# Kernel tuning notes

Measured on AMD Instinct MI355X. Metric: run time of the kernel, lower is better.

## Reference

```python
import jax, jax.numpy as jnp
import numpy as np

N_NODES = 10000
N_EDGES = 320000
IN_DIM = 256
HID = 64
HEADS = 4
OUT_DIM = 64
NEG_SLOPE = 0.2


def setup_inputs() -> dict:
    key = jax.random.key(0)
    ks = jax.random.split(key, 10)
    s = 0.05
    return {
        "h": jax.random.normal(ks[0], (N_NODES, IN_DIM), jnp.float32),
        "src": jax.random.randint(ks[1], (N_EDGES,), 0, N_NODES, jnp.int32),
        "dst": jax.random.randint(ks[2], (N_EDGES,), 0, N_NODES, jnp.int32),
        "W1": jax.random.normal(ks[3], (IN_DIM, HEADS * HID), jnp.float32) * s,
        "al1": jax.random.normal(ks[4], (HEADS, HID), jnp.float32) * s,
        "ar1": jax.random.normal(ks[5], (HEADS, HID), jnp.float32) * s,
        "b1": jnp.zeros((HEADS * HID,), jnp.float32),
        "W2": jax.random.normal(ks[6], (HEADS * HID, OUT_DIM), jnp.float32) * s,
        "al2": jax.random.normal(ks[7], (1, OUT_DIM), jnp.float32) * s,
        "ar2": jax.random.normal(ks[8], (1, OUT_DIM), jnp.float32) * s,
        "b2": jnp.zeros((OUT_DIM,), jnp.float32),
    }


def _gatconv(h, W, al, ar, b, src, dst, n_heads, d_out):
    """DGL-style GATConv: project, edge-softmax attention, scatter-aggregate."""
    n = h.shape[0]
    feat = (h @ W).reshape(n, n_heads, d_out)          # [N,H,D]
    el = jnp.sum(feat * al, axis=-1)                   # [N,H]
    er = jnp.sum(feat * ar, axis=-1)                   # [N,H]
    e = jax.nn.leaky_relu(el[src] + er[dst], NEG_SLOPE)  # [E,H]
    # segment softmax over incoming edges of each dst node
    m = jax.ops.segment_max(e, dst, num_segments=n)    # [N,H]
    ex = jnp.exp(e - m[dst])                           # [E,H]
    denom = jax.ops.segment_sum(ex, dst, num_segments=n)  # [N,H]
    alpha = ex / denom[dst]                            # [E,H]
    msg = feat[src] * alpha[:, :, None]                # [E,H,D]
    out = jax.ops.segment_sum(msg, dst, num_segments=n)  # [N,H,D]
    return out + b.reshape(n_heads, d_out)


def reference(h, src, dst, W1, al1, ar1, b1, W2, al2, ar2, b2):
    h1 = _gatconv(h, W1, al1, ar1, b1, src, dst, HEADS, HID)
    h1 = jax.nn.elu(h1.reshape(N_NODES, HEADS * HID))  # flatten(1) then ELU
    h2 = _gatconv(h1, W2, al2, ar2, b2, src, dst, 1, OUT_DIM)
    return jnp.squeeze(h2, axis=1)  # [N, OUT_DIM]
```

## Files before the change

kernel.cpp:

```cpp
#include <hip/hip_runtime.h>
#include <hip/hip_bf16.h>
#include <stdint.h>

#define NN 10000
#define NE 320000
#define NH 4
#define BCAP 128

#define GEMM1_MB 79
#define GEMM1_BLOCKS (GEMM1_MB * 4)
#define BUILD_BLOCKS 1250

typedef __attribute__((ext_vector_type(8))) short s16x8;
typedef __attribute__((ext_vector_type(4))) float f32x4;
typedef __attribute__((ext_vector_type(8))) unsigned short u16x8;

static __device__ __forceinline__ float b2f(unsigned short u) {
    union { unsigned int i; float f; } x; x.i = ((unsigned int)u) << 16; return x.f;
}
static __device__ __forceinline__ unsigned short f2b(float f) {
    unsigned int u = __float_as_uint(f);
    unsigned int r = (u + 0x7fffu + ((u >> 16) & 1u)) >> 16;
    return (unsigned short)r;
}

__global__ __launch_bounds__(256) void k_prep(const unsigned short* __restrict__ hraw,
                        const void* __restrict__ W1, const void* __restrict__ W2,
                        const void* al1, const void* ar1, const void* b1,
                        const void* al2, const void* ar2, const void* b2,
                        unsigned short* __restrict__ W1T, unsigned short* __restrict__ W2T,
                        unsigned short* __restrict__ canon, int* __restrict__ cnt,
                        int* __restrict__ flag) {
    __shared__ int sb[256];
    int t = threadIdx.x;
    int c = 0;
    for (int i = t; i < 2048; i += 256) {
        unsigned short u = hraw[i];
        int e = (u >> 7) & 0xFF;
        c += (e >= 97 && e <= 157) ? 1 : 0;
    }
    sb[t] = c;
    __syncthreads();
    for (int o = 128; o > 0; o >>= 1) {
        if (t < o) sb[t] += sb[t + o];
        __syncthreads();
    }
    int isbf = (sb[0] >= 1741) ? 1 : 0;

    int idx = blockIdx.x * 256 + t;
    if (idx < 65536) {
        int n = idx >> 8, k = idx & 255;
        W1T[idx] = isbf ? ((const unsigned short*)W1)[k * 256 + n]
                        : f2b(((const float*)W1)[k * 256 + n]);
    } else if (idx < 81920) {
        int j = idx - 65536;
        int n = j >> 8, k = j & 255;
        W2T[j] = isbf ? ((const unsigned short*)W2)[k * 64 + n]
                      : f2b(((const float*)W2)[k * 64 + n]);
    } else if (idx < 82880) {
        int j = idx - 81920;
        const void* srcp; int q;
        if      (j < 256) { srcp = al1; q = j; }
        else if (j < 512) { srcp = ar1; q = j - 256; }
        else if (j < 768) { srcp = b1;  q = j - 512; }
        else if (j < 832) { srcp = al2; q = j - 768; }
        else if (j < 896) { srcp = ar2; q = j - 832; }
        else              { srcp = b2;  q = j - 896; }
        canon[j] = isbf ? ((const unsigned short*)srcp)[q] : f2b(((const float*)srcp)[q]);
    } else if (idx < 92880) {
        cnt[idx - 82880] = 0;
    } else if (idx == 92880) {
        flag[0] = isbf;
    }
}

#define BSTRIDE 264
static __device__ __forceinline__ void gemm_body(short* Bs,
                        const void* __restrict__ A, const unsigned short* __restrict__ BT,
                        unsigned short* __restrict__ C,
                        float* __restrict__ el, float* __restrict__ er,
                        const unsigned short* __restrict__ al,
                        const unsigned short* __restrict__ ar,
                        int M, int N, int H, int a_isbf, int mtile, int head) {
    int t = threadIdx.x;
    int wave = t >> 6, lane = t & 63;
    int m0 = mtile * 128;
    const unsigned short* Bh = BT + (size_t)head * 64 * 256;

#pragma unroll
    for (int i = 0; i < 8; ++i) {
        int idx = t + i * 256;
        int row = idx >> 5, chunk = idx & 31;
        *(s16x8*)&Bs[row * BSTRIDE + chunk * 8] =
            *(const s16x8*)&Bh[(size_t)row * 256 + chunk * 8];
    }
    __syncthreads();

    int kq = (lane >> 4) * 8;
    const unsigned short* Ab = (const unsigned short*)A;
    const float*          Af = (const float*)A;
    int aR[2];
#pragma unroll
    for (int mi = 0; mi < 2; ++mi) {
        int aRow = m0 + mi * 64 + wave * 16 + (lane & 15);
        aR[mi] = (aRow < M) ? aRow : M - 1;
    }
    f32x4 acc[2][4] = {};

#pragma unroll
    for (int k0 = 0; k0 < 256; k0 += 32) {
        s16x8 afr[2];
#pragma unroll
        for (int mi = 0; mi < 2; ++mi) {
            if (a_isbf) {
                afr[mi] = *(const s16x8*)&Ab[(size_t)aR[mi] * 256 + k0 + kq];
            } else {
                const float* pf = &Af[(size_t)aR[mi] * 256 + k0 + kq];
                float4 x0 = *(const float4*)pf;
                float4 x1 = *(const float4*)(pf + 4);
                afr[mi][0] = (short)f2b(x0.x); afr[mi][1] = (short)f2b(x0.y);
                afr[mi][2] = (short)f2b(x0.z); afr[mi][3] = (short)f2b(x0.w);
                afr[mi][4] = (short)f2b(x1.x); afr[mi][5] = (short)f2b(x1.y);
                afr[mi][6] = (short)f2b(x1.z); afr[mi][7] = (short)f2b(x1.w);
            }
        }
#pragma unroll
        for (int nt = 0; nt < 4; ++nt) {
            s16x8 bfr = *(const s16x8*)&Bs[(nt * 16 + (lane & 15)) * BSTRIDE + k0 + kq];
            acc[0][nt] = __builtin_amdgcn_mfma_f32_16x16x32_bf16(afr[0], bfr, acc[0][nt], 0, 0, 0);
            acc[1][nt] = __builtin_amdgcn_mfma_f32_16x16x32_bf16(afr[1], bfr, acc[1][nt], 0, 0, 0);
        }
    }

    float alv[4], arv[4];
#pragma unroll
    for (int nt = 0; nt < 4; ++nt) {
        int c = (lane & 15) + nt * 16;
        alv[nt] = b2f(al[head * 64 + c]);
        arv[nt] = b2f(ar[head * 64 + c]);
    }
    int col0 = head * 64 + (lane & 15);
#pragma unroll
    for (int mi = 0; mi < 2; ++mi) {
        int r0 = m0 + mi * 64 + wave * 16 + (lane >> 4) * 4;
        float cr[4][4];
#pragma unroll
        for (int nt = 0; nt < 4; ++nt) {
            int col = col0 + nt * 16;
#pragma unroll
            for (int i = 0; i < 4; ++i) {
                unsigned short cb = f2b(acc[mi][nt][i]);
                cr[nt][i] = b2f(cb);
                int r = r0 + i;
                if (r < M) C[(size_t)r * N + col] = cb;
            }
        }
#pragma unroll
        for (int i = 0; i < 4; ++i) {
            float pl = 0.f, pr = 0.f;
#pragma unroll
            for (int nt = 0; nt < 4; ++nt) {
                pl += cr[nt][i] * alv[nt];
                pr += cr[nt][i] * arv[nt];
            }
#pragma unroll
            for (int o = 1; o < 16; o <<= 1) {
                pl += __shfl_xor(pl, o, 64);
                pr += __shfl_xor(pr, o, 64);
            }
            int r = r0 + i;
            if ((lane & 15) == 0 && r < M) {
                el[(size_t)r * H + head] = pl;
                er[(size_t)r * H + head] = pr;
            }
        }
    }
}

__global__ __launch_bounds__(256) void k_g1b(const void* __restrict__ A,
                        const unsigned short* __restrict__ W1T,
                        unsigned short* __restrict__ feat1,
                        float* __restrict__ el, float* __restrict__ er,
                        const unsigned short* __restrict__ al,
                        const unsigned short* __restrict__ ar,
                        const int* __restrict__ flagp,
                        const int* __restrict__ src, const int* __restrict__ dst,
                        int* __restrict__ cnt, int* __restrict__ bucket) {
    __shared__ short Bs[64 * BSTRIDE];
    int bid = blockIdx.x;
    if (bid < GEMM1_BLOCKS) {
        int head = bid / GEMM1_MB;
        int mtile = bid - head * GEMM1_MB;
        gemm_body(Bs, A, W1T, feat1, el, er, al, ar, NN, 256, NH, flagp[0], mtile, head);
    } else {
        int i = (bid - GEMM1_BLOCKS) * 256 + threadIdx.x;
        if (i < NE) {
            int d = dst[i];
            int pos = atomicAdd(&cnt[d], 1);
            if (pos < BCAP) bucket[(d << 7) + pos] = src[i];
        }
    }
}

__global__ __launch_bounds__(256) void k_gemm(const void* __restrict__ A,
                                              const unsigned short* __restrict__ BT,
                                              unsigned short* __restrict__ C,
                                              float* __restrict__ el, float* __restrict__ er,
                                              const unsigned short* __restrict__ al,
                                              const unsigned short* __restrict__ ar,
                                              int M, int N, int H) {
    __shared__ short Bs[64 * BSTRIDE];
    gemm_body(Bs, A, BT, C, el, er, al, ar, M, N, H, 1, blockIdx.x, blockIdx.y);
}

__global__ __launch_bounds__(256) void k_edge1(const int* __restrict__ cnt,
                        const int* __restrict__ bucket,
                        const float* __restrict__ el, const float* __restrict__ er,
                        const unsigned short* __restrict__ feat,
                        const unsigned short* __restrict__ b1,
                        unsigned short* __restrict__ h1) {
    int wave = threadIdx.x >> 6, lane = threadIdx.x & 63;
    int node = blockIdx.x * 4 + wave;
    if (node >= NN) return;
    int eg = lane >> 3, d8 = lane & 7;
    int end = cnt[node]; if (end > BCAP) end = BCAP;
    const int* bkt = bucket + ((size_t)node << 7);
    float4 er4 = *(const float4*)&er[(size_t)node * 4];

    if (end <= 64) {
        int s = 0;
        float w0 = 0.f, w1 = 0.f, w2 = 0.f, w3 = 0.f;
        if (lane < end) {
            s = bkt[lane];
            float4 el4 = *(const float4*)&el[(size_t)s * 4];
            float x0 = el4.x + er4.x; x0 = (x0 >= 0.f) ? x0 : 0.2f * x0;
            float x1 = el4.y + er4.y; x1 = (x1 >= 0.f) ? x1 : 0.2f * x1;
            float x2 = el4.z + er4.z; x2 = (x2 >= 0.f) ? x2 : 0.2f * x2;
            float x3 = el4.w + er4.w; x3 = (x3 >= 0.f) ? x3 : 0.2f * x3;
            w0 = __expf(x0); w1 = __expf(x1);
            w2 = __expf(x2); w3 = __expf(x3);
        }
        int niter = (end + 7) >> 3;
#pragma unroll
        for (int h = 0; h < 4; ++h) {
            float wh = (h == 0) ? w0 : (h == 1) ? w1 : (h == 2) ? w2 : w3;
            float a[8] = {};
            for (int i = 0; i < niter; ++i) {
                int idx = 8 * i + eg;
                float we = __shfl(wh, idx, 64);
                int   se = __shfl(s, idx, 64);
                u16x8 fv = *(const u16x8*)&feat[(((size_t)se * NH + h) << 6) + (d8 << 3)];
#pragma unroll
                for (int j = 0; j < 8; ++j) a[j] += we * b2f(fv[j]);
            }
            float ls = wh;
#pragma unroll
            for (int o = 1; o < 64; o <<= 1) ls += __shfl_xor(ls, o, 64);
#pragma unroll
            for (int j = 0; j < 8; ++j) {
                a[j] += __shfl_xor(a[j], 8, 64);
                a[j] += __shfl_xor(a[j], 16, 64);
                a[j] += __shfl_xor(a[j], 32, 64);
            }
            if (eg == 0) {
                float inv = (ls > 0.f) ? 1.f / ls : 0.f;
                u16x8 r;
#pragma unroll
                for (int j = 0; j < 8; ++j) {
                    float o = a[j] * inv + b2f(b1[h * 64 + d8 * 8 + j]);
                    o = (o > 0.f) ? o : (__expf(o) - 1.f);
                    r[j] = f2b(o);
                }
                *(u16x8*)&h1[(((size_t)node * NH + h) << 6) + d8 * 8] = r;
            }
        }
    } else {
        float a[4][8] = {};
        float ls0 = 0.f, ls1 = 0.f, ls2 = 0.f, ls3 = 0.f;
        for (int base = 0; base < end; base += 64) {
            int c = base + lane;
            int s = 0;
            float w0 = 0.f, w1 = 0.f, w2 = 0.f, w3 = 0.f;
            if (c < end) {
                s = bkt[c];
                float4 el4 = *(const float4*)&el[(size_t)s * 4];
                float x0 = el4.x + er4.x; x0 = (x0 >= 0.f) ? x0 : 0.2f * x0;
                float x1 = el4.y + er4.y; x1 = (x1 >= 0.f) ? x1 : 0.2f * x1;
                float x2 = el4.z + er4.z; x2 = (x2 >= 0.f) ? x2 : 0.2f * x2;
                float x3 = el4.w + er4.w; x3 = (x3 >= 0.f) ? x3 : 0.2f * x3;
                w0 = __expf(x0); w1 = __expf(x1);
                w2 = __expf(x2); w3 = __expf(x3);
            }
            ls0 += w0; ls1 += w1; ls2 += w2; ls3 += w3;
            int cn = end - base; if (cn > 64) cn = 64;
            int niter = (cn + 7) >> 3;
#pragma unroll
            for (int h = 0; h < 4; ++h) {
                float wh = (h == 0) ? w0 : (h == 1) ? w1 : (h == 2) ? w2 : w3;
                for (int i = 0; i < niter; ++i) {
                    int idx = 8 * i + eg;
                    float we = __shfl(wh, idx, 64);
                    int   se = __shfl(s, idx, 64);
                    u16x8 fv = *(const u16x8*)&feat[(((size_t)se * NH + h) << 6) + (d8 << 3)];
#pragma unroll
                    for (int j = 0; j < 8; ++j) a[h][j] += we * b2f(fv[j]);
                }
            }
        }
#pragma unroll
        for (int h = 0; h < 4; ++h) {
            float ls = (h == 0) ? ls0 : (h == 1) ? ls1 : (h == 2) ? ls2 : ls3;
#pragma unroll
            for (int o = 1; o < 64; o <<= 1) ls += __shfl_xor(ls, o, 64);
#pragma unroll
            for (int j = 0; j < 8; ++j) {
                a[h][j] += __shfl_xor(a[h][j], 8, 64);
                a[h][j] += __shfl_xor(a[h][j], 16, 64);
                a[h][j] += __shfl_xor(a[h][j], 32, 64);
            }
            if (eg == 0) {
                float inv = (ls > 0.f) ? 1.f / ls : 0.f;
                u16x8 r;
#pragma unroll
                for (int j = 0; j < 8; ++j) {
                    float o = a[h][j] * inv + b2f(b1[h * 64 + d8 * 8 + j]);
                    o = (o > 0.f) ? o : (__expf(o) - 1.f);
                    r[j] = f2b(o);
                }
                *(u16x8*)&h1[(((size_t)node * NH + h) << 6) + d8 * 8] = r;
            }
        }
    }
}

__global__ __launch_bounds__(256) void k_edge2(const int* __restrict__ cnt,
                        const int* __restrict__ bucket,
                        const float* __restrict__ el, const float* __restrict__ er,
                        const unsigned short* __restrict__ feat,
                        const unsigned short* __restrict__ b2,
                        void* __restrict__ out, const int* __restrict__ flagp) {
    int wave = threadIdx.x >> 6, lane = threadIdx.x & 63;
    int node = blockIdx.x * 4 + wave;
    if (node >= NN) return;
    int eg = lane >> 3, d8 = lane & 7;
    int isbf = flagp[0];
    int end = cnt[node]; if (end > BCAP) end = BCAP;
    const int* bkt = bucket + ((size_t)node << 7);
    float er_d = er[node];
    float lsum = 0.f;
    float a[8] = {};
    for (int base = 0; base < end; base += 64) {
        int c = base + lane;
        float wgt = 0.f; int s = 0;
        if (c < end) {
            s = bkt[c];
            float x = el[s] + er_d;
            x = (x >= 0.f) ? x : 0.2f * x;
            wgt = __expf(x);
        }
        lsum += wgt;
        int cn = end - base; if (cn > 64) cn = 64;
        int niter = (cn + 7) >> 3;
#pragma unroll 2
        for (int i = 0; i < niter; ++i) {
            int idx = 8 * i + eg;
            float we = __shfl(wgt, idx, 64);
            int   se = __shfl(s, idx, 64);
            u16x8 fv = *(const u16x8*)&feat[((size_t)se << 6) + (d8 << 3)];
#pragma unroll
            for (int j = 0; j < 8; ++j) a[j] += we * b2f(fv[j]);
        }
    }
#pragma unroll
    for (int o = 1; o < 64; o <<= 1) lsum += __shfl_xor(lsum, o, 64);
#pragma unroll
    for (int j = 0; j < 8; ++j) {
        a[j] += __shfl_xor(a[j], 8, 64);
        a[j] += __shfl_xor(a[j], 16, 64);
        a[j] += __shfl_xor(a[j], 32, 64);
    }
    if (eg == 0) {
        float inv = (lsum > 0.f) ? 1.f / lsum : 0.f;
        float o[8];
#pragma unroll
        for (int j = 0; j < 8; ++j) o[j] = a[j] * inv + b2f(b2[d8 * 8 + j]);
        size_t ob = ((size_t)node << 6) + d8 * 8;
        if (isbf) {
            u16x8 r;
#pragma unroll
            for (int j = 0; j < 8; ++j) r[j] = f2b(o[j]);
            *(u16x8*)&((unsigned short*)out)[ob] = r;
        } else {
            float4 r0, r1;
            r0.x = o[0]; r0.y = o[1]; r0.z = o[2]; r0.w = o[3];
            r1.x = o[4]; r1.y = o[5]; r1.z = o[6]; r1.w = o[7];
            *(float4*)&((float*)out)[ob] = r0;
            *(float4*)&((float*)out)[ob + 4] = r1;
        }
    }
}

extern "C" void kernel_launch(void* const* d_in, const int* in_sizes, int n_in,
                              void* d_out, int out_size, void* d_ws, size_t ws_size,
                              hipStream_t stream) {
    const void* h   = d_in[0];
    const int*  src = (const int*)d_in[1];
    const int*  dst = (const int*)d_in[2];
    const void* W1  = d_in[3];
    const void* al1 = d_in[4];
    const void* ar1 = d_in[5];
    const void* b1  = d_in[6];
    const void* W2  = d_in[7];
    const void* al2 = d_in[8];
    const void* ar2 = d_in[9];
    const void* b2  = d_in[10];

    char* w = (char*)d_ws;
    size_t off = 0;
    auto alloc = [&](size_t bytes) -> void* {
        void* p = w + off;
        off = (off + bytes + 255) & ~(size_t)255;
        return p;
    };
    int* flag               = (int*)alloc(8);
    int* cnt                = (int*)alloc(NN * 4);
    int* bucket             = (int*)alloc((size_t)NN * BCAP * 4);
    unsigned short* canon   = (unsigned short*)alloc(960 * 2);
    unsigned short* W1T     = (unsigned short*)alloc(256 * 256 * 2);
    unsigned short* W2T     = (unsigned short*)alloc(64 * 256 * 2);
    unsigned short* feat1   = (unsigned short*)alloc((size_t)NN * 256 * 2);
    float* el1              = (float*)alloc(NN * NH * 4);
    float* er1              = (float*)alloc(NN * NH * 4);
    unsigned short* h1      = (unsigned short*)alloc((size_t)NN * 256 * 2);
    unsigned short* feat2   = (unsigned short*)alloc((size_t)NN * 64 * 2);
    float* el2              = (float*)alloc(NN * 4);
    float* er2              = (float*)alloc(NN * 4);
    (void)ws_size; (void)in_sizes; (void)n_in; (void)out_size;

    unsigned short* cal1 = canon + 0;
    unsigned short* car1 = canon + 256;
    unsigned short* cb1  = canon + 512;
    unsigned short* cal2 = canon + 768;
    unsigned short* car2 = canon + 832;
    unsigned short* cb2  = canon + 896;

    k_prep<<<363, 256, 0, stream>>>((const unsigned short*)h, W1, W2,
                                    al1, ar1, b1, al2, ar2, b2,
                                    W1T, W2T, canon, cnt, flag);
    k_g1b<<<GEMM1_BLOCKS + BUILD_BLOCKS, 256, 0, stream>>>(h, W1T, feat1, el1, er1,
                                                           cal1, car1, flag,
                                                           src, dst, cnt, bucket);
    k_edge1<<<(NN + 3) / 4, 256, 0, stream>>>(cnt, bucket, el1, er1, feat1, cb1, h1);
    k_gemm<<<dim3(GEMM1_MB, 1), 256, 0, stream>>>(h1, W2T, feat2, el2, er2,
                                                  cal2, car2, NN, 64, 1);
    k_edge2<<<(NN + 3) / 4, 256, 0, stream>>>(cnt, bucket, el2, er2, feat2, cb2, d_out, flag);
}
```

Before: 157.9 us.

## Split layer-1 aggregation per head and halve GEMM row tiles for more parallelism

Replaces the per-node layer-1 edge kernel, which looped over all four heads in one wave, with a kernel that launches one wave per (node, head) pair, giving four times as many waves and fewer accumulator registers per wave. The GEMM tile shrinks from 128 to 64 rows, doubling the block count for both GEMMs. The layer-2 edge kernel gains a single-chunk fast path for nodes with at most 64 incoming edges, plus occupancy hints. In exchange, each edge's source index and per-edge weight are now computed once per head instead of once per node, and el/er are read with a stride of four floats.

```diff
diff --git a/kernel.cpp b/kernel.cpp
--- a/kernel.cpp
+++ b/kernel.cpp
@@ -7,8 +7,8 @@
 #define NH 4
 #define BCAP 128
 
-#define GEMM1_MB 79
-#define GEMM1_BLOCKS (GEMM1_MB * 4)
+#define GEMM1_MT 157
+#define GEMM1_BLOCKS (GEMM1_MT * 4)
 #define BUILD_BLOCKS 1250
 
 typedef __attribute__((ext_vector_type(8))) short s16x8;
@@ -84,7 +84,7 @@
                         int M, int N, int H, int a_isbf, int mtile, int head) {
     int t = threadIdx.x;
     int wave = t >> 6, lane = t & 63;
-    int m0 = mtile * 128;
+    int m0 = mtile * 64;
     const unsigned short* Bh = BT + (size_t)head * 64 * 256;
 
 #pragma unroll
@@ -99,36 +99,28 @@
     int kq = (lane >> 4) * 8;
     const unsigned short* Ab = (const unsigned short*)A;
     const float*          Af = (const float*)A;
-    int aR[2];
-#pragma unroll
-    for (int mi = 0; mi < 2; ++mi) {
-        int aRow = m0 + mi * 64 + wave * 16 + (lane & 15);
-        aR[mi] = (aRow < M) ? aRow : M - 1;
-    }
-    f32x4 acc[2][4] = {};
+    int aRow = m0 + wave * 16 + (lane & 15);
+    int aR = (aRow < M) ? aRow : M - 1;
+    f32x4 acc[4] = {};
 
 #pragma unroll
     for (int k0 = 0; k0 < 256; k0 += 32) {
-        s16x8 afr[2];
-#pragma unroll
-        for (int mi = 0; mi < 2; ++mi) {
-            if (a_isbf) {
-                afr[mi] = *(const s16x8*)&Ab[(size_t)aR[mi] * 256 + k0 + kq];
-            } else {
-                const float* pf = &Af[(size_t)aR[mi] * 256 + k0 + kq];
-                float4 x0 = *(const float4*)pf;
-                float4 x1 = *(const float4*)(pf + 4);
-                afr[mi][0] = (short)f2b(x0.x); afr[mi][1] = (short)f2b(x0.y);
-                afr[mi][2] = (short)f2b(x0.z); afr[mi][3] = (short)f2b(x0.w);
-                afr[mi][4] = (short)f2b(x1.x); afr[mi][5] = (short)f2b(x1.y);
-                afr[mi][6] = (short)f2b(x1.z); afr[mi][7] = (short)f2b(x1.w);
-            }
+        s16x8 afr;
+        if (a_isbf) {
+            afr = *(const s16x8*)&Ab[(size_t)aR * 256 + k0 + kq];
+        } else {
+            const float* pf = &Af[(size_t)aR * 256 + k0 + kq];
+            float4 x0 = *(const float4*)pf;
+            float4 x1 = *(const float4*)(pf + 4);
+            afr[0] = (short)f2b(x0.x); afr[1] = (short)f2b(x0.y);
+            afr[2] = (short)f2b(x0.z); afr[3] = (short)f2b(x0.w);
+            afr[4] = (short)f2b(x1.x); afr[5] = (short)f2b(x1.y);
+            afr[6] = (short)f2b(x1.z); afr[7] = (short)f2b(x1.w);
         }
 #pragma unroll
         for (int nt = 0; nt < 4; ++nt) {
             s16x8 bfr = *(const s16x8*)&Bs[(nt * 16 + (lane & 15)) * BSTRIDE + k0 + kq];
-            acc[0][nt] = __builtin_amdgcn_mfma_f32_16x16x32_bf16(afr[0], bfr, acc[0][nt], 0, 0, 0);
-            acc[1][nt] = __builtin_amdgcn_mfma_f32_16x16x32_bf16(afr[1], bfr, acc[1][nt], 0, 0, 0);
+            acc[nt] = __builtin_amdgcn_mfma_f32_16x16x32_bf16(afr, bfr, acc[nt], 0, 0, 0);
         }
     }
 
@@ -140,39 +132,36 @@
         arv[nt] = b2f(ar[head * 64 + c]);
     }
     int col0 = head * 64 + (lane & 15);
-#pragma unroll
-    for (int mi = 0; mi < 2; ++mi) {
-        int r0 = m0 + mi * 64 + wave * 16 + (lane >> 4) * 4;
-        float cr[4][4];
+    int r0 = m0 + wave * 16 + (lane >> 4) * 4;
+    float cr[4][4];
+#pragma unroll
+    for (int nt = 0; nt < 4; ++nt) {
+        int col = col0 + nt * 16;
+#pragma unroll
+        for (int i = 0; i < 4; ++i) {
+            unsigned short cb = f2b(acc[nt][i]);
+            cr[nt][i] = b2f(cb);
+            int r = r0 + i;
+            if (r < M) C[(size_t)r * N + col] = cb;
+        }
+    }
+#pragma unroll
+    for (int i = 0; i < 4; ++i) {
+        float pl = 0.f, pr = 0.f;
 #pragma unroll
         for (int nt = 0; nt < 4; ++nt) {
-            int col = col0 + nt * 16;
-#pragma unroll
-            for (int i = 0; i < 4; ++i) {
-                unsigned short cb = f2b(acc[mi][nt][i]);
-                cr[nt][i] = b2f(cb);
-                int r = r0 + i;
-                if (r < M) C[(size_t)r * N + col] = cb;
-            }
-        }
-#pragma unroll
-        for (int i = 0; i < 4; ++i) {
-            float pl = 0.f, pr = 0.f;
-#pragma unroll
-            for (int nt = 0; nt < 4; ++nt) {
-                pl += cr[nt][i] * alv[nt];
-                pr += cr[nt][i] * arv[nt];
-            }
-#pragma unroll
-            for (int o = 1; o < 16; o <<= 1) {
-                pl += __shfl_xor(pl, o, 64);
-                pr += __shfl_xor(pr, o, 64);
-            }
-            int r = r0 + i;
-            if ((lane & 15) == 0 && r < M) {
-                el[(size_t)r * H + head] = pl;
-                er[(size_t)r * H + head] = pr;
-            }
+            pl += cr[nt][i] * alv[nt];
+            pr += cr[nt][i] * arv[nt];
+        }
+#pragma unroll
+        for (int o = 1; o < 16; o <<= 1) {
+            pl += __shfl_xor(pl, o, 64);
+            pr += __shfl_xor(pr, o, 64);
+        }
+        int r = r0 + i;
+        if ((lane & 15) == 0 && r < M) {
+            el[(size_t)r * H + head] = pl;
+            er[(size_t)r * H + head] = pr;
         }
     }
 }
@@ -189,8 +178,8 @@
     __shared__ short Bs[64 * BSTRIDE];
     int bid = blockIdx.x;
     if (bid < GEMM1_BLOCKS) {
-        int head = bid / GEMM1_MB;
-        int mtile = bid - head * GEMM1_MB;
+        int head = bid / GEMM1_MT;
+        int mtile = bid - head * GEMM1_MT;
         gemm_body(Bs, A, W1T, feat1, el, er, al, ar, NN, 256, NH, flagp[0], mtile, head);
     } else {
         int i = (bid - GEMM1_BLOCKS) * 256 + threadIdx.x;
@@ -198,6 +187,107 @@
             int d = dst[i];
             int pos = atomicAdd(&cnt[d], 1);
             if (pos < BCAP) bucket[(d << 7) + pos] = src[i];
+        }
+    }
+}
+
+__global__ __launch_bounds__(256, 8) void k_e1h(const int* __restrict__ cnt,
+                        const int* __restrict__ bucket,
+                        const float* __restrict__ el, const float* __restrict__ er,
+                        const unsigned short* __restrict__ feat,
+                        const unsigned short* __restrict__ b1,
+                        unsigned short* __restrict__ h1) {
+    int wave = threadIdx.x >> 6, lane = threadIdx.x & 63;
+    int bid = blockIdx.x;
+    int head = bid / 2500;
+    int node = (bid - head * 2500) * 4 + wave;
+    int eg = lane >> 3, d8 = lane & 7;
+    int end = cnt[node]; if (end > BCAP) end = BCAP;
+    const int* bkt = bucket + ((size_t)node << 7);
+    float er_d = er[(size_t)node * 4 + head];
+
+    if (end <= 64) {
+        int s = 0; float w = 0.f;
+        if (lane < end) {
+            s = bkt[lane];
+            float x = el[(size_t)s * 4 + head] + er_d;
+            x = (x >= 0.f) ? x : 0.2f * x;
+            w = __expf(x);
+        }
+        float ls = w;
+#pragma unroll
+        for (int o = 1; o < 64; o <<= 1) ls += __shfl_xor(ls, o, 64);
+        float a[8] = {};
+        int niter = (end + 7) >> 3;
+#pragma unroll 4
+        for (int i = 0; i < niter; ++i) {
+            int idx = 8 * i + eg;
+            int   se = __shfl(s, idx, 64);
+            float we = __shfl(w, idx, 64);
+            u16x8 fv = *(const u16x8*)&feat[(((size_t)se * NH + head) << 6) + (d8 << 3)];
+#pragma unroll
+            for (int j = 0; j < 8; ++j) a[j] += we * b2f(fv[j]);
+        }
+#pragma unroll
+        for (int j = 0; j < 8; ++j) {
+            a[j] += __shfl_xor(a[j], 8, 64);
+            a[j] += __shfl_xor(a[j], 16, 64);
+            a[j] += __shfl_xor(a[j], 32, 64);
+        }
+        if (eg == 0) {
+            float inv = (ls > 0.f) ? 1.f / ls : 0.f;
+            u16x8 r;
+#pragma unroll
+            for (int j = 0; j < 8; ++j) {
+                float o = a[j] * inv + b2f(b1[head * 64 + d8 * 8 + j]);
+                o = (o > 0.f) ? o : (__expf(o) - 1.f);
+                r[j] = f2b(o);
+            }
+            *(u16x8*)&h1[(((size_t)node * NH + head) << 6) + d8 * 8] = r;
+        }
+    } else {
+        float a[8] = {};
+        float ls = 0.f;
+        for (int base = 0; base < end; base += 64) {
+            int c = base + lane;
+            int s = 0; float w = 0.f;
+            if (c < end) {
+                s = bkt[c];
+                float x = el[(size_t)s * 4 + head] + er_d;
+                x = (x >= 0.f) ? x : 0.2f * x;
+                w = __expf(x);
+            }
+            ls += w;
+            int cn = end - base; if (cn > 64) cn = 64;
+            int niter = (cn + 7) >> 3;
+#pragma unroll 2
+            for (int i = 0; i < niter; ++i) {
+                int idx = 8 * i + eg;
+                int   se = __shfl(s, idx, 64);
+                float we = __shfl(w, idx, 64);
+                u16x8 fv = *(const u16x8*)&feat[(((size_t)se * NH + head) << 6) + (d8 << 3)];
+#pragma unroll
+                for (int j = 0; j < 8; ++j) a[j] += we * b2f(fv[j]);
+            }
+        }
+#pragma unroll
+        for (int o = 1; o < 64; o <<= 1) ls += __shfl_xor(ls, o, 64);
+#pragma unroll
+        for (int j = 0; j < 8; ++j) {
+            a[j] += __shfl_xor(a[j], 8, 64);
+            a[j] += __shfl_xor(a[j], 16, 64);
+            a[j] += __shfl_xor(a[j], 32, 64);
+        }
+        if (eg == 0) {
+            float inv = (ls > 0.f) ? 1.f / ls : 0.f;
+            u16x8 r;
+#pragma unroll
+            for (int j = 0; j < 8; ++j) {
+                float o = a[j] * inv + b2f(b1[head * 64 + d8 * 8 + j]);
+                o = (o > 0.f) ? o : (__expf(o) - 1.f);
+                r[j] = f2b(o);
+            }
+            *(u16x8*)&h1[(((size_t)node * NH + head) << 6) + d8 * 8] = r;
         }
     }
 }
@@ -213,127 +303,7 @@
     gemm_body(Bs, A, BT, C, el, er, al, ar, M, N, H, 1, blockIdx.x, blockIdx.y);
 }
 
-__global__ __launch_bounds__(256) void k_edge1(const int* __restrict__ cnt,
-                        const int* __restrict__ bucket,
-                        const float* __restrict__ el, const float* __restrict__ er,
-                        const unsigned short* __restrict__ feat,
-                        const unsigned short* __restrict__ b1,
-                        unsigned short* __restrict__ h1) {
-    int wave = threadIdx.x >> 6, lane = threadIdx.x & 63;
-    int node = blockIdx.x * 4 + wave;
-    if (node >= NN) return;
-    int eg = lane >> 3, d8 = lane & 7;
-    int end = cnt[node]; if (end > BCAP) end = BCAP;
-    const int* bkt = bucket + ((size_t)node << 7);
-    float4 er4 = *(const float4*)&er[(size_t)node * 4];
-
-    if (end <= 64) {
-        int s = 0;
-        float w0 = 0.f, w1 = 0.f, w2 = 0.f, w3 = 0.f;
-        if (lane < end) {
-            s = bkt[lane];
-            float4 el4 = *(const float4*)&el[(size_t)s * 4];
-            float x0 = el4.x + er4.x; x0 = (x0 >= 0.f) ? x0 : 0.2f * x0;
-            float x1 = el4.y + er4.y; x1 = (x1 >= 0.f) ? x1 : 0.2f * x1;
-            float x2 = el4.z + er4.z; x2 = (x2 >= 0.f) ? x2 : 0.2f * x2;
-            float x3 = el4.w + er4.w; x3 = (x3 >= 0.f) ? x3 : 0.2f * x3;
-            w0 = __expf(x0); w1 = __expf(x1);
-            w2 = __expf(x2); w3 = __expf(x3);
-        }
-        int niter = (end + 7) >> 3;
-#pragma unroll
-        for (int h = 0; h < 4; ++h) {
-            float wh = (h == 0) ? w0 : (h == 1) ? w1 : (h == 2) ? w2 : w3;
-            float a[8] = {};
-            for (int i = 0; i < niter; ++i) {
-                int idx = 8 * i + eg;
-                float we = __shfl(wh, idx, 64);
-                int   se = __shfl(s, idx, 64);
-                u16x8 fv = *(const u16x8*)&feat[(((size_t)se * NH + h) << 6) + (d8 << 3)];
-#pragma unroll
-                for (int j = 0; j < 8; ++j) a[j] += we * b2f(fv[j]);
-            }
-            float ls = wh;
-#pragma unroll
-            for (int o = 1; o < 64; o <<= 1) ls += __shfl_xor(ls, o, 64);
-#pragma unroll
-            for (int j = 0; j < 8; ++j) {
-                a[j] += __shfl_xor(a[j], 8, 64);
-                a[j] += __shfl_xor(a[j], 16, 64);
-                a[j] += __shfl_xor(a[j], 32, 64);
-            }
-            if (eg == 0) {
-                float inv = (ls > 0.f) ? 1.f / ls : 0.f;
-                u16x8 r;
-#pragma unroll
-                for (int j = 0; j < 8; ++j) {
-                    float o = a[j] * inv + b2f(b1[h * 64 + d8 * 8 + j]);
-                    o = (o > 0.f) ? o : (__expf(o) - 1.f);
-                    r[j] = f2b(o);
-                }
-                *(u16x8*)&h1[(((size_t)node * NH + h) << 6) + d8 * 8] = r;
-            }
-        }
-    } else {
-        float a[4][8] = {};
-        float ls0 = 0.f, ls1 = 0.f, ls2 = 0.f, ls3 = 0.f;
-        for (int base = 0; base < end; base += 64) {
-            int c = base + lane;
-            int s = 0;
-            float w0 = 0.f, w1 = 0.f, w2 = 0.f, w3 = 0.f;
-            if (c < end) {
-                s = bkt[c];
-                float4 el4 = *(const float4*)&el[(size_t)s * 4];
-                float x0 = el4.x + er4.x; x0 = (x0 >= 0.f) ? x0 : 0.2f * x0;
-                float x1 = el4.y + er4.y; x1 = (x1 >= 0.f) ? x1 : 0.2f * x1;
-                float x2 = el4.z + er4.z; x2 = (x2 >= 0.f) ? x2 : 0.2f * x2;
-                float x3 = el4.w + er4.w; x3 = (x3 >= 0.f) ? x3 : 0.2f * x3;
-                w0 = __expf(x0); w1 = __expf(x1);
-                w2 = __expf(x2); w3 = __expf(x3);
-            }
-            ls0 += w0; ls1 += w1; ls2 += w2; ls3 += w3;
-            int cn = end - base; if (cn > 64) cn = 64;
-            int niter = (cn + 7) >> 3;
-#pragma unroll
-            for (int h = 0; h < 4; ++h) {
-                float wh = (h == 0) ? w0 : (h == 1) ? w1 : (h == 2) ? w2 : w3;
-                for (int i = 0; i < niter; ++i) {
-                    int idx = 8 * i + eg;
-                    float we = __shfl(wh, idx, 64);
-                    int   se = __shfl(s, idx, 64);
-                    u16x8 fv = *(const u16x8*)&feat[(((size_t)se * NH + h) << 6) + (d8 << 3)];
-#pragma unroll
-                    for (int j = 0; j < 8; ++j) a[h][j] += we * b2f(fv[j]);
-                }
-            }
-        }
-#pragma unroll
-        for (int h = 0; h < 4; ++h) {
-            float ls = (h == 0) ? ls0 : (h == 1) ? ls1 : (h == 2) ? ls2 : ls3;
-#pragma unroll
-            for (int o = 1; o < 64; o <<= 1) ls += __shfl_xor(ls, o, 64);
-#pragma unroll
-            for (int j = 0; j < 8; ++j) {
-                a[h][j] += __shfl_xor(a[h][j], 8, 64);
-                a[h][j] += __shfl_xor(a[h][j], 16, 64);
-                a[h][j] += __shfl_xor(a[h][j], 32, 64);
-            }
-            if (eg == 0) {
-                float inv = (ls > 0.f) ? 1.f / ls : 0.f;
-                u16x8 r;
-#pragma unroll
-                for (int j = 0; j < 8; ++j) {
-                    float o = a[h][j] * inv + b2f(b1[h * 64 + d8 * 8 + j]);
-                    o = (o > 0.f) ? o : (__expf(o) - 1.f);
-                    r[j] = f2b(o);
-                }
-                *(u16x8*)&h1[(((size_t)node * NH + h) << 6) + d8 * 8] = r;
-            }
-        }
-    }
-}
-
-__global__ __launch_bounds__(256) void k_edge2(const int* __restrict__ cnt,
+__global__ __launch_bounds__(256, 4) void k_edge2(const int* __restrict__ cnt,
                         const int* __restrict__ bucket,
                         const float* __restrict__ el, const float* __restrict__ er,
                         const unsigned short* __restrict__ feat,
@@ -347,21 +317,20 @@
     int end = cnt[node]; if (end > BCAP) end = BCAP;
     const int* bkt = bucket + ((size_t)node << 7);
     float er_d = er[node];
-    float lsum = 0.f;
+    float lsum;
     float a[8] = {};
-    for (int base = 0; base < end; base += 64) {
-        int c = base + lane;
-        float wgt = 0.f; int s = 0;
-        if (c < end) {
-            s = bkt[c];
+
+    if (end <= 64) {
+        int s = 0; float wgt = 0.f;
+        if (lane < end) {
+            s = bkt[lane];
             float x = el[s] + er_d;
             x = (x >= 0.f) ? x : 0.2f * x;
             wgt = __expf(x);
         }
-        lsum += wgt;
-        int cn = end - base; if (cn > 64) cn = 64;
-        int niter = (cn + 7) >> 3;
-#pragma unroll 2
+        lsum = wgt;
+        int niter = (end + 7) >> 3;
+#pragma unroll 4
         for (int i = 0; i < niter; ++i) {
             int idx = 8 * i + eg;
             float we = __shfl(wgt, idx, 64);
@@ -369,6 +338,30 @@
             u16x8 fv = *(const u16x8*)&feat[((size_t)se << 6) + (d8 << 3)];
 #pragma unroll
             for (int j = 0; j < 8; ++j) a[j] += we * b2f(fv[j]);
+        }
+    } else {
+        lsum = 0.f;
+        for (int base = 0; base < end; base += 64) {
+            int c = base + lane;
+            float wgt = 0.f; int s = 0;
+            if (c < end) {
+                s = bkt[c];
+                float x = el[s] + er_d;
+                x = (x >= 0.f) ? x : 0.2f * x;
+                wgt = __expf(x);
+            }
+            lsum += wgt;
+            int cn = end - base; if (cn > 64) cn = 64;
+            int niter = (cn + 7) >> 3;
+#pragma unroll 2
+            for (int i = 0; i < niter; ++i) {
+                int idx = 8 * i + eg;
+                float we = __shfl(wgt, idx, 64);
+                int   se = __shfl(s, idx, 64);
+                u16x8 fv = *(const u16x8*)&feat[((size_t)se << 6) + (d8 << 3)];
+#pragma unroll
+                for (int j = 0; j < 8; ++j) a[j] += we * b2f(fv[j]);
+            }
         }
     }
 #pragma unroll
@@ -450,8 +443,8 @@
     k_g1b<<<GEMM1_BLOCKS + BUILD_BLOCKS, 256, 0, stream>>>(h, W1T, feat1, el1, er1,
                                                            cal1, car1, flag,
                                                            src, dst, cnt, bucket);
-    k_edge1<<<(NN + 3) / 4, 256, 0, stream>>>(cnt, bucket, el1, er1, feat1, cb1, h1);
-    k_gemm<<<dim3(GEMM1_MB, 1), 256, 0, stream>>>(h1, W2T, feat2, el2, er2,
+    k_e1h<<<NN, 256, 0, stream>>>(cnt, bucket, el1, er1, feat1, cb1, h1);
+    k_gemm<<<dim3(GEMM1_MT, 1), 256, 0, stream>>>(h1, W2T, feat2, el2, er2,
                                                   cal2, car2, NN, 64, 1);
     k_edge2<<<(NN + 3) / 4, 256, 0, stream>>>(cnt, bucket, el2, er2, feat2, cb2, d_out, flag);
 }
```

New measurement: 148.3 us. -6.1%, faster.
